# Kernel optimization log

Measured on AMD Instinct MI355X. Metric: run time of the kernel, lower is better.

The kernel has to match this reference:

```python
import jax, jax.numpy as jnp
import numpy as np
from jax import lax

DN = ('NCHW', 'OIHW', 'NCHW')
SAME = ((1, 1), (1, 1))
VALID = ((0, 0), (0, 0))


def conv(x, w, pad):
    return lax.conv_general_dilated(x, w, (1, 1), pad, dimension_numbers=DN)


def convT(x, w, strides):
    # inverse (transposed) conv; for kernel==stride this exactly inverts the
    # non-overlapping pooling rulebook used by spconv's SparseInverseConv2d
    return lax.conv_transpose(x, w, strides, 'VALID', dimension_numbers=DN)


def maxpool(x, k):
    return lax.reduce_window(x, -jnp.inf, lax.max, (1, 1) + k, (1, 1) + k, 'VALID')


def lrelu(x):
    return jnp.where(x >= 0, x, 0.01 * x)  # F.leaky_relu default slope


def setup_inputs() -> dict:
    key = jax.random.key(0)
    ks = jax.random.split(key, 14)
    B, C, H, W = 32, 6, 500, 128
    x = jax.random.normal(ks[0], (B, C, H, W), jnp.float32)  # fully dense => all voxels active

    def p(k, shape):
        return jax.random.normal(k, shape, jnp.float32) * 0.05

    return {
        'x': x,
        'w1': p(ks[1], (8, 6, 3, 3)),      # SubMConv2d 6->8
        'w2': p(ks[2], (16, 8, 3, 3)),     # SubMConv2d 8->16
        'w3': p(ks[3], (32, 16, 3, 3)),    # SubMConv2d 16->32
        'wmu': p(ks[4], (1, 32, 1, 5)),    # SparseConv2d 32->1, kernel (1,5)
        'wlv': p(ks[5], (1, 32, 1, 5)),
        'wu0': p(ks[6], (32, 1, 1, 5)),    # SparseInverseConv2d 1->32
        'wu1': p(ks[7], (32, 32, 5, 2)),   # inverse of pool3
        'w4': p(ks[8], (16, 32, 3, 3)),
        'wu2': p(ks[9], (16, 16, 5, 2)),   # inverse of pool2
        'w5': p(ks[10], (8, 16, 3, 3)),
        'wu3': p(ks[11], (8, 8, 2, 2)),    # inverse of pool1
        'w6': p(ks[12], (6, 8, 3, 3)),
    }


def reference(x, w1, w2, w3, wmu, wlv, wu0, wu1, w4, wu2, w5, wu3, w6):
    B = x.shape[0]
    # ---- encoder ----
    h = lrelu(conv(x, w1, SAME))        # [B,8,500,128]
    h = maxpool(h, (2, 2))              # [B,8,250,64]
    h = lrelu(conv(h, w2, SAME))        # [B,16,250,64]
    h = maxpool(h, (5, 2))              # [B,16,50,32]
    h = lrelu(conv(h, w3, SAME))        # [B,32,50,32]
    h = maxpool(h, (5, 2))              # [B,32,10,16]
    mu = conv(h, wmu, VALID)            # [B,1,10,12]
    logvar = conv(h, wlv, VALID)        # [B,1,10,12]
    # ---- reparameterise ----
    eps = jax.random.normal(jax.random.key(42), mu.shape, mu.dtype)
    z = mu + eps * jnp.exp(0.5 * logvar)
    # ---- decoder ----
    d = lrelu(convT(z, wu0, (1, 1)))    # [B,32,10,16]
    d = lrelu(convT(d, wu1, (5, 2)))    # [B,32,50,32]
    d = lrelu(conv(d, w4, SAME))        # [B,16,50,32]
    d = lrelu(convT(d, wu2, (5, 2)))    # [B,16,250,64]
    d = lrelu(conv(d, w5, SAME))        # [B,8,250,64]
    d = lrelu(convT(d, wu3, (2, 2)))    # [B,8,500,128]
    d = lrelu(conv(d, w6, SAME))        # [B,6,500,128]
    return (d, mu.reshape(B, -1), logvar.reshape(B, -1), z.reshape(B, -1))
```

## Files before the change

### kernel.cpp

```cpp
#include <hip/hip_runtime.h>
#include <stdint.h>

#define DI __device__ __forceinline__

DI float lrelu(float x){ return x >= 0.0f ? x : 0.01f*x; }

DI uint32_t rotl32(uint32_t x, int d){ return (x << d) | (x >> (32 - d)); }

DI void threefry_0_42(uint32_t& x0, uint32_t& x1){
  const uint32_t ks0 = 0u, ks1 = 42u, ks2 = 0x1BD11BF0u;
  x0 += ks0; x1 += ks1;
  #define TFR(d) { x0 += x1; x1 = rotl32(x1,(d)); x1 ^= x0; }
  TFR(13) TFR(15) TFR(26) TFR(6)  x0 += ks1; x1 += ks2 + 1u;
  TFR(17) TFR(29) TFR(16) TFR(24) x0 += ks2; x1 += ks0 + 2u;
  TFR(13) TFR(15) TFR(26) TFR(6)  x0 += ks0; x1 += ks1 + 3u;
  TFR(17) TFR(29) TFR(16) TFR(24) x0 += ks1; x1 += ks2 + 4u;
  TFR(13) TFR(15) TFR(26) TFR(6)  x0 += ks2; x1 += ks0 + 5u;
  #undef TFR
}

DI float erfinv_f32(float x){
  float w = -log1pf(-x*x);
  float p;
  if (w < 5.0f){
    w = w - 2.5f;
    p = 2.81022636e-08f;
    p = fmaf(p, w, 3.43273939e-07f);
    p = fmaf(p, w, -3.5233877e-06f);
    p = fmaf(p, w, -4.39150654e-06f);
    p = fmaf(p, w, 0.00021858087f);
    p = fmaf(p, w, -0.00125372503f);
    p = fmaf(p, w, -0.00417768164f);
    p = fmaf(p, w, 0.246640727f);
    p = fmaf(p, w, 1.50140941f);
  } else {
    w = sqrtf(w) - 3.0f;
    p = -0.000200214257f;
    p = fmaf(p, w, 0.000100950558f);
    p = fmaf(p, w, 0.00134934322f);
    p = fmaf(p, w, -0.00367342844f);
    p = fmaf(p, w, 0.00573950773f);
    p = fmaf(p, w, -0.0076224613f);
    p = fmaf(p, w, 0.00943887047f);
    p = fmaf(p, w, 1.00167406f);
    p = fmaf(p, w, 2.83297682f);
  }
  return p * x;
}

#define OUT_D_OFF   0
#define OUT_MU_OFF  12288000
#define OUT_LV_OFF  (12288000 + 3840)
#define OUT_Z_OFF   (12288000 + 7680)

__global__ __launch_bounds__(256) void k_enc1(const float* __restrict__ x,
                                              const float* __restrict__ w1,
                                              float* __restrict__ p1){
  __shared__ float tile[6*10*130];
  int tid = threadIdx.x;
  int band = blockIdx.x % 63;
  int b    = blockIdx.x / 63;
  int r0 = band*8;
  for (int idx = tid; idx < 6*10*130; idx += 256){
    int lc = idx % 130;
    int rest = idx / 130;
    int lr = rest % 10;
    int ch = rest / 10;
    int gr = r0 - 1 + lr, gc = lc - 1;
    float v = 0.0f;
    if ((unsigned)gr < 500u && (unsigned)gc < 128u)
      v = x[((b*6+ch)*500+gr)*128+gc];
    tile[idx] = v;
  }
  __syncthreads();
  int pw = tid & 63, pr = tid >> 6;
  int ph = band*4 + pr;
  float acc[2][2][8];
  #pragma unroll
  for (int a=0;a<2;a++)
    #pragma unroll
    for (int d=0;d<2;d++)
      #pragma unroll
      for (int o=0;o<8;o++) acc[a][d][o] = 0.0f;
  int base = (2*pr)*130 + 2*pw;
  #pragma unroll 2
  for (int c = 0; c < 6; ++c){
    float win[4][4];
    #pragma unroll
    for (int i=0;i<4;i++)
      #pragma unroll
      for (int j=0;j<4;j++)
        win[i][j] = tile[c*1300 + base + i*130 + j];
    #pragma unroll
    for (int kh=0;kh<3;kh++)
      #pragma unroll
      for (int kw=0;kw<3;kw++){
        float wv[8];
        #pragma unroll
        for (int o=0;o<8;o++) wv[o] = w1[((o*6+c)*3+kh)*3+kw];
        #pragma unroll
        for (int dy=0;dy<2;dy++)
          #pragma unroll
          for (int dx=0;dx<2;dx++){
            float v = win[dy+kh][dx+kw];
            #pragma unroll
            for (int o=0;o<8;o++) acc[dy][dx][o] = fmaf(v, wv[o], acc[dy][dx][o]);
          }
      }
  }
  if (ph < 250){
    #pragma unroll
    for (int o=0;o<8;o++){
      float m = fmaxf(fmaxf(acc[0][0][o], acc[0][1][o]), fmaxf(acc[1][0][o], acc[1][1][o]));
      p1[((b*8+o)*250+ph)*64+pw] = lrelu(m);
    }
  }
}

__global__ __launch_bounds__(256) void k_enc2(const float* __restrict__ in,
                                              const float* __restrict__ w2,
                                              float* __restrict__ p2){
  __shared__ float tile[8*22*66];
  int tid = threadIdx.x;
  int band = blockIdx.x % 13;
  int b    = blockIdx.x / 13;
  int r0 = band*20;
  for (int idx = tid; idx < 8*22*66; idx += 256){
    int lc = idx % 66;
    int rest = idx / 66;
    int lr = rest % 22;
    int ch = rest / 22;
    int gr = r0 - 1 + lr, gc = lc - 1;
    float v = 0.0f;
    if ((unsigned)gr < 250u && (unsigned)gc < 64u)
      v = in[((b*8+ch)*250+gr)*64+gc];
    tile[idx] = v;
  }
  __syncthreads();
  int dx = tid & 1; int u = tid >> 1;
  int pw = u & 31; int pr = (u >> 5) & 3;
  int cw = 2*pw + dx;
  int ph = band*4 + pr;
  float acc[5][16];
  #pragma unroll
  for (int dy=0;dy<5;dy++)
    #pragma unroll
    for (int o=0;o<16;o++) acc[dy][o] = 0.0f;
  int base = (5*pr)*66 + cw;
  #pragma unroll 1
  for (int c = 0; c < 8; ++c){
    float win[7][3];
    #pragma unroll
    for (int i=0;i<7;i++)
      #pragma unroll
      for (int j=0;j<3;j++)
        win[i][j] = tile[c*1452 + base + i*66 + j];
    #pragma unroll
    for (int kh=0;kh<3;kh++)
      #pragma unroll
      for (int kw=0;kw<3;kw++){
        float wv[16];
        #pragma unroll
        for (int o=0;o<16;o++) wv[o] = w2[((o*8+c)*3+kh)*3+kw];
        #pragma unroll
        for (int dy=0;dy<5;dy++){
          float v = win[dy+kh][kw];
          #pragma unroll
          for (int o=0;o<16;o++) acc[dy][o] = fmaf(v, wv[o], acc[dy][o]);
        }
      }
  }
  #pragma unroll
  for (int o=0;o<16;o++){
    float m = acc[0][o];
    #pragma unroll
    for (int dy=1;dy<5;dy++) m = fmaxf(m, acc[dy][o]);
    m = fmaxf(m, __shfl_xor(m, 1));
    if (dx == 0 && ph < 50) p2[((b*16+o)*50+ph)*32+pw] = lrelu(m);
  }
}

__global__ __launch_bounds__(256) void k_conv3(const float* __restrict__ in,
                                               const float* __restrict__ w3,
                                               float* __restrict__ outp){
  __shared__ float tile[16*10*34];
  int tid = threadIdx.x;
  int bi = blockIdx.x;
  int band = bi % 7; int oh = (bi/7) & 1; int b = bi / 14;
  int r0 = band*8;
  for (int idx = tid; idx < 16*10*34; idx += 256){
    int lc = idx % 34;
    int rest = idx / 34;
    int lr = rest % 10;
    int ch = rest / 10;
    int gr = r0 - 1 + lr, gc = lc - 1;
    float v = 0.0f;
    if ((unsigned)gr < 50u && (unsigned)gc < 32u)
      v = in[((b*16+ch)*50+gr)*32+gc];
    tile[idx] = v;
  }
  __syncthreads();
  int col = tid & 31, tr = tid >> 5;
  int h = r0 + tr;
  float acc[16];
  #pragma unroll
  for (int o=0;o<16;o++) acc[o] = 0.0f;
  int base = tr*34 + col;
  #pragma unroll 2
  for (int c = 0; c < 16; ++c){
    float win[3][3];
    #pragma unroll
    for (int i=0;i<3;i++)
      #pragma unroll
      for (int j=0;j<3;j++)
        win[i][j] = tile[c*340 + base + i*34 + j];
    #pragma unroll
    for (int kh=0;kh<3;kh++)
      #pragma unroll
      for (int kw=0;kw<3;kw++){
        float v = win[kh][kw];
        #pragma unroll
        for (int o=0;o<16;o++)
          acc[o] = fmaf(v, w3[(((oh*16+o)*16+c)*3+kh)*3+kw], acc[o]);
      }
  }
  if (h < 50){
    #pragma unroll
    for (int o=0;o<16;o++)
      outp[((b*32 + oh*16 + o)*50 + h)*32 + col] = lrelu(acc[o]);
  }
}

__global__ __launch_bounds__(256) void k_pool3(const float* __restrict__ in,
                                               float* __restrict__ outp){
  int t = blockIdx.x*256 + threadIdx.x;
  int pw = t & 15; int u = t >> 4; int ph = u % 10; u /= 10; int o = u & 31; int b = u >> 5;
  float m = -INFINITY;
  #pragma unroll
  for (int dh=0;dh<5;dh++)
    #pragma unroll
    for (int dw=0;dw<2;dw++)
      m = fmaxf(m, in[((b*32+o)*50 + 5*ph+dh)*32 + 2*pw+dw]);
  outp[((b*32+o)*10+ph)*16+pw] = m;
}

__global__ __launch_bounds__(256) void k_latent(const float* __restrict__ p3,
                                                const float* __restrict__ wmu,
                                                const float* __restrict__ wlv,
                                                float* __restrict__ outp){
  int t = blockIdx.x*256 + threadIdx.x;
  int w = t % 12; int h = (t/12) % 10; int b = t/120;
  float mu = 0.0f, lv = 0.0f;
  for (int c = 0; c < 32; ++c){
    const float* row = p3 + ((b*32+c)*10+h)*16 + w;
    #pragma unroll
    for (int kw=0;kw<5;kw++){
      float v = row[kw];
      mu = fmaf(v, wmu[c*5+kw], mu);
      lv = fmaf(v, wlv[c*5+kw], lv);
    }
  }
  uint32_t x0 = 0u, x1 = (uint32_t)t;
  threefry_0_42(x0, x1);
  uint32_t bits = x0 ^ x1;
  float f = __uint_as_float((bits >> 9) | 0x3f800000u) - 1.0f;
  const float lo = -0.99999994f;
  float uu = fmaxf(lo, f * 2.0f + lo);
  float eps = 1.41421356f * erfinv_f32(uu);
  float z = mu + eps * expf(0.5f * lv);
  outp[OUT_MU_OFF + t] = mu;
  outp[OUT_LV_OFF + t] = lv;
  outp[OUT_Z_OFF  + t] = z;
}

__global__ __launch_bounds__(256) void k_dec0(const float* __restrict__ outp,
                                              const float* __restrict__ wu0,
                                              float* __restrict__ d0){
  int t = blockIdx.x*256 + threadIdx.x;
  int w = t & 15; int u = t >> 4; int h = u % 10; u /= 10; int o = u & 31; int b = u >> 5;
  const float* z = outp + OUT_Z_OFF;
  float a = 0.0f;
  #pragma unroll
  for (int kw=0;kw<5;kw++){
    int ww = w + kw - 4;
    if ((unsigned)ww < 12u) a = fmaf(z[b*120 + h*12 + ww], wu0[o*5+kw], a);
  }
  d0[((b*32+o)*10+h)*16+w] = lrelu(a);
}

__global__ __launch_bounds__(256) void k_dec1(const float* __restrict__ d0,
                                              const float* __restrict__ wu1,
                                              float* __restrict__ d1){
  int t = blockIdx.x*256 + threadIdx.x;
  int wo = t & 31; int u = t >> 5; int ho = u % 50; u /= 50; int og = u & 3; int b = u >> 2;
  int i = ho / 5, r = ho - 5*i, jj = wo >> 1, s = wo & 1;
  const float* ip = d0 + b*5120 + i*16 + jj;
  float in[32];
  #pragma unroll
  for (int c=0;c<32;c++) in[c] = ip[c*160];
  #pragma unroll
  for (int oo=0;oo<8;oo++){
    int o = og*8 + oo;
    const float* wp = wu1 + (o*32*5 + (4-r))*2 + (1-s);
    float a = 0.0f;
    #pragma unroll
    for (int c=0;c<32;c++) a = fmaf(in[c], wp[c*10], a);
    d1[((b*32+o)*50+ho)*32+wo] = lrelu(a);
  }
}

__global__ __launch_bounds__(256) void k_c4(const float* __restrict__ in,
                                            const float* __restrict__ w4,
                                            float* __restrict__ outp){
  __shared__ float tile[32*10*34];
  int tid = threadIdx.x;
  int bi = blockIdx.x;
  int band = bi % 7; int oh = (bi/7) & 1; int b = bi / 14;
  int r0 = band*8;
  for (int idx = tid; idx < 32*10*34; idx += 256){
    int lc = idx % 34;
    int rest = idx / 34;
    int lr = rest % 10;
    int ch = rest / 10;
    int gr = r0 - 1 + lr, gc = lc - 1;
    float v = 0.0f;
    if ((unsigned)gr < 50u && (unsigned)gc < 32u)
      v = in[((b*32+ch)*50+gr)*32+gc];
    tile[idx] = v;
  }
  __syncthreads();
  int col = tid & 31, tr = tid >> 5;
  int h = r0 + tr;
  float acc[8];
  #pragma unroll
  for (int o=0;o<8;o++) acc[o] = 0.0f;
  int base = tr*34 + col;
  #pragma unroll 2
  for (int c = 0; c < 32; ++c){
    float win[3][3];
    #pragma unroll
    for (int i=0;i<3;i++)
      #pragma unroll
      for (int j=0;j<3;j++)
        win[i][j] = tile[c*340 + base + i*34 + j];
    #pragma unroll
    for (int kh=0;kh<3;kh++)
      #pragma unroll
      for (int kw=0;kw<3;kw++){
        float v = win[kh][kw];
        #pragma unroll
        for (int o=0;o<8;o++)
          acc[o] = fmaf(v, w4[(((oh*8+o)*32+c)*3+kh)*3+kw], acc[o]);
      }
  }
  if (h < 50){
    #pragma unroll
    for (int o=0;o<8;o++)
      outp[((b*16 + oh*8 + o)*50 + h)*32 + col] = lrelu(acc[o]);
  }
}

__global__ __launch_bounds__(256) void k_u2(const float* __restrict__ d2,
                                            const float* __restrict__ wu2,
                                            float* __restrict__ d3){
  int t = blockIdx.x*256 + threadIdx.x;
  int w = t & 63; int u = t >> 6; int h = u % 250; int b = u / 250;
  int i = h / 5, r = h - 5*i, jj = w >> 1, s = w & 1;
  const float* ip = d2 + b*25600 + i*32 + jj;
  float in[16];
  #pragma unroll
  for (int c=0;c<16;c++) in[c] = ip[c*1600];
  #pragma unroll
  for (int o=0;o<16;o++){
    const float* wp = wu2 + (o*16*5 + (4-r))*2 + (1-s);
    float a = 0.0f;
    #pragma unroll
    for (int c=0;c<16;c++) a = fmaf(in[c], wp[c*10], a);
    d3[((b*16+o)*250+h)*64+w] = lrelu(a);
  }
}

__global__ __launch_bounds__(256) void k_c5(const float* __restrict__ in,
                                            const float* __restrict__ w5,
                                            float* __restrict__ outp){
  __shared__ float tile[16*10*66];
  int tid = threadIdx.x;
  int band = blockIdx.x % 32;
  int b    = blockIdx.x / 32;
  int r0 = band*8;
  for (int idx = tid; idx < 16*10*66; idx += 256){
    int lc = idx % 66;
    int rest = idx / 66;
    int lr = rest % 10;
    int ch = rest / 10;
    int gr = r0 - 1 + lr, gc = lc - 1;
    float v = 0.0f;
    if ((unsigned)gr < 250u && (unsigned)gc < 64u)
      v = in[((b*16+ch)*250+gr)*64+gc];
    tile[idx] = v;
  }
  __syncthreads();
  int cp = tid & 31, tr = tid >> 5;
  int h = r0 + tr;
  float acc[2][8];
  #pragma unroll
  for (int dx=0;dx<2;dx++)
    #pragma unroll
    for (int o=0;o<8;o++) acc[dx][o] = 0.0f;
  int base = tr*66 + 2*cp;
  #pragma unroll 2
  for (int c = 0; c < 16; ++c){
    float win[3][4];
    #pragma unroll
    for (int i=0;i<3;i++)
      #pragma unroll
      for (int j=0;j<4;j++)
        win[i][j] = tile[c*660 + base + i*66 + j];
    #pragma unroll
    for (int kh=0;kh<3;kh++)
      #pragma unroll
      for (int kw=0;kw<3;kw++){
        float wv[8];
        #pragma unroll
        for (int o=0;o<8;o++) wv[o] = w5[((o*16+c)*3+kh)*3+kw];
        #pragma unroll
        for (int dx=0;dx<2;dx++){
          float v = win[kh][dx+kw];
          #pragma unroll
          for (int o=0;o<8;o++) acc[dx][o] = fmaf(v, wv[o], acc[dx][o]);
        }
      }
  }
  if (h < 250){
    #pragma unroll
    for (int dx=0;dx<2;dx++)
      #pragma unroll
      for (int o=0;o<8;o++)
        outp[((b*8+o)*250+h)*64 + 2*cp+dx] = lrelu(acc[dx][o]);
  }
}

__global__ __launch_bounds__(256) void k_u3c6(const float* __restrict__ d4,
                                              const float* __restrict__ wu3,
                                              const float* __restrict__ w6,
                                              float* __restrict__ outp){
  __shared__ __align__(16) float dt[8*10*132];
  __shared__ __align__(16) float wl[256];
  int tid = threadIdx.x;
  int band = blockIdx.x % 63;
  int b    = blockIdx.x / 63;
  int r0 = band*8;
  wl[tid] = wu3[tid];
  if (tid < 80){
    int ch = tid / 10, lr = tid % 10;
    dt[(ch*10+lr)*132 + 128] = 0.0f;
    dt[(ch*10+lr)*132 + 129] = 0.0f;
  }
  __syncthreads();
  for (int s = tid; s < 320; s += 256){
    int q = s & 31, lr = s >> 5;
    int h = r0 - 1 + lr;
    if ((unsigned)h < 500u){
      int i2 = h >> 1, r = h & 1;
      float2 dv[8];
      #pragma unroll
      for (int c=0;c<8;c++)
        dv[c] = *(const float2*)(d4 + ((b*8+c)*250 + i2)*64 + 2*q);
      int wbase = (1-r)*2;
      #pragma unroll
      for (int o5=0;o5<8;o5++){
        float a0=0.f,a1=0.f,a2=0.f,a3=0.f;
        #pragma unroll
        for (int c=0;c<8;c++){
          float2 wp = *(const float2*)(wl + o5*32 + c*4 + wbase);
          a0 = fmaf(dv[c].x, wp.y, a0);
          a1 = fmaf(dv[c].x, wp.x, a1);
          a2 = fmaf(dv[c].y, wp.y, a2);
          a3 = fmaf(dv[c].y, wp.x, a3);
        }
        float4 v4 = make_float4(lrelu(a0), lrelu(a1), lrelu(a2), lrelu(a3));
        *(float4*)(dt + (o5*10+lr)*132 + 4*q) = v4;
      }
    } else {
      float4 z = make_float4(0.f,0.f,0.f,0.f);
      #pragma unroll
      for (int o5=0;o5<8;o5++)
        *(float4*)(dt + (o5*10+lr)*132 + 4*q) = z;
    }
  }
  __syncthreads();
  int q = tid & 31, tr = tid >> 5;
  int R = r0 + tr;
  float acc[4][6];
  #pragma unroll
  for (int j=0;j<4;j++)
    #pragma unroll
    for (int o=0;o<6;o++) acc[j][o] = 0.0f;
  int left = (q==0) ? 129 : (4*q - 1);
  #pragma unroll 2
  for (int ch=0; ch<8; ++ch){
    #pragma unroll
    for (int wr=0; wr<3; ++wr){
      const float* row = dt + (ch*10 + tr + wr)*132;
      float win[6];
      float4 m = *(const float4*)(row + 4*q);
      win[0] = row[left];
      win[1] = m.x; win[2] = m.y; win[3] = m.z; win[4] = m.w;
      win[5] = row[4*q + 4];
      #pragma unroll
      for (int kw=0;kw<3;kw++){
        #pragma unroll
        for (int o=0;o<6;o++){
          float wv = w6[((o*8+ch)*3+wr)*3+kw];
          #pragma unroll
          for (int j=0;j<4;j++)
            acc[j][o] = fmaf(win[j+kw], wv, acc[j][o]);
        }
      }
    }
  }
  if (R < 500){
    #pragma unroll
    for (int o=0;o<6;o++){
      float4 v = make_float4(lrelu(acc[0][o]), lrelu(acc[1][o]),
                             lrelu(acc[2][o]), lrelu(acc[3][o]));
      *(float4*)(outp + ((b*6+o)*500 + R)*128 + 4*q) = v;
    }
  }
}

extern "C" void kernel_launch(void* const* d_in, const int* in_sizes, int n_in,
                              void* d_out, int out_size, void* d_ws, size_t ws_size,
                              hipStream_t stream){
  const float* x   = (const float*)d_in[0];
  const float* w1  = (const float*)d_in[1];
  const float* w2  = (const float*)d_in[2];
  const float* w3  = (const float*)d_in[3];
  const float* wmu = (const float*)d_in[4];
  const float* wlv = (const float*)d_in[5];
  const float* wu0 = (const float*)d_in[6];
  const float* wu1 = (const float*)d_in[7];
  const float* w4  = (const float*)d_in[8];
  const float* wu2 = (const float*)d_in[9];
  const float* w5  = (const float*)d_in[10];
  const float* wu3 = (const float*)d_in[11];
  const float* w6  = (const float*)d_in[12];
  float* out = (float*)d_out;
  float* A  = (float*)d_ws;
  float* Bb = A + 4096000;

  k_enc1 <<<2016, 256, 0, stream>>>(x,  w1,  A);
  k_enc2 <<< 416, 256, 0, stream>>>(A,  w2,  Bb);
  k_conv3<<< 448, 256, 0, stream>>>(Bb, w3,  A);
  k_pool3<<< 640, 256, 0, stream>>>(A,  Bb);
  k_latent<<< 15, 256, 0, stream>>>(Bb, wmu, wlv, out);
  k_dec0 <<< 640, 256, 0, stream>>>(out, wu0, A);
  k_dec1 <<< 800, 256, 0, stream>>>(A,  wu1, Bb);
  k_c4   <<< 448, 256, 0, stream>>>(Bb, w4,  A);
  k_u2   <<<2000, 256, 0, stream>>>(A,  wu2, Bb);
  k_c5   <<<1024, 256, 0, stream>>>(Bb, w5,  A);
  k_u3c6 <<<2016, 256, 0, stream>>>(A, wu3, w6, out);
}
```

Measured before the change: 381.0 us.

## Fuse pool3/latent/dec0/dec1 and u2 into c5; retile enc2 for more blocks

Merges pool3, the latent/reparameterisation step, dec0 and dec1 into one per-batch kernel that keeps its intermediates in shared memory. Also computes the u2 transposed conv inside the c5 tile load, so the large d3 intermediate is never written to or read from global memory. enc2 is retiled to 10-row bands with two output-channel groups, giving 800 blocks instead of 416. The fused latent kernel runs only 32 blocks with about 80KB of shared memory, so it may underuse the GPU. The u2c5 kernel also recomputes halo rows of u2.

```diff
diff --git a/kernel.cpp b/kernel.cpp
--- a/kernel.cpp
+++ b/kernel.cpp
@@ -120,63 +120,65 @@
 __global__ __launch_bounds__(256) void k_enc2(const float* __restrict__ in,
                                               const float* __restrict__ w2,
                                               float* __restrict__ p2){
-  __shared__ float tile[8*22*66];
+  __shared__ float tile[8*12*66];
   int tid = threadIdx.x;
-  int band = blockIdx.x % 13;
-  int b    = blockIdx.x / 13;
-  int r0 = band*20;
-  for (int idx = tid; idx < 8*22*66; idx += 256){
+  int band = blockIdx.x % 25;
+  int b    = blockIdx.x / 25;
+  int cr0 = band*10;
+  for (int idx = tid; idx < 8*12*66; idx += 256){
     int lc = idx % 66;
     int rest = idx / 66;
-    int lr = rest % 22;
-    int ch = rest / 22;
-    int gr = r0 - 1 + lr, gc = lc - 1;
+    int lr = rest % 12;
+    int ch = rest / 12;
+    int gr = cr0 - 1 + lr, gc = lc - 1;
     float v = 0.0f;
     if ((unsigned)gr < 250u && (unsigned)gc < 64u)
       v = in[((b*8+ch)*250+gr)*64+gc];
     tile[idx] = v;
   }
   __syncthreads();
-  int dx = tid & 1; int u = tid >> 1;
-  int pw = u & 31; int pr = (u >> 5) & 3;
+  int dx = tid & 1;
+  int pw = (tid >> 1) & 31;
+  int pr = (tid >> 6) & 1;
+  int og = tid >> 7;
   int cw = 2*pw + dx;
-  int ph = band*4 + pr;
-  float acc[5][16];
+  int ph = band*2 + pr;
+  float acc[5][8];
   #pragma unroll
   for (int dy=0;dy<5;dy++)
     #pragma unroll
-    for (int o=0;o<16;o++) acc[dy][o] = 0.0f;
+    for (int oo=0;oo<8;oo++) acc[dy][oo] = 0.0f;
   int base = (5*pr)*66 + cw;
-  #pragma unroll 1
+  #pragma unroll 2
   for (int c = 0; c < 8; ++c){
     float win[7][3];
     #pragma unroll
     for (int i=0;i<7;i++)
       #pragma unroll
       for (int j=0;j<3;j++)
-        win[i][j] = tile[c*1452 + base + i*66 + j];
+        win[i][j] = tile[c*792 + base + i*66 + j];
     #pragma unroll
     for (int kh=0;kh<3;kh++)
       #pragma unroll
       for (int kw=0;kw<3;kw++){
-        float wv[16];
-        #pragma unroll
-        for (int o=0;o<16;o++) wv[o] = w2[((o*8+c)*3+kh)*3+kw];
+        float wv[8];
+        #pragma unroll
+        for (int oo=0;oo<8;oo++) wv[oo] = w2[(((og*8+oo)*8+c)*3+kh)*3+kw];
         #pragma unroll
         for (int dy=0;dy<5;dy++){
           float v = win[dy+kh][kw];
           #pragma unroll
-          for (int o=0;o<16;o++) acc[dy][o] = fmaf(v, wv[o], acc[dy][o]);
+          for (int oo=0;oo<8;oo++) acc[dy][oo] = fmaf(v, wv[oo], acc[dy][oo]);
         }
       }
   }
   #pragma unroll
-  for (int o=0;o<16;o++){
-    float m = acc[0][o];
-    #pragma unroll
-    for (int dy=1;dy<5;dy++) m = fmaxf(m, acc[dy][o]);
+  for (int oo=0;oo<8;oo++){
+    float m = acc[0][oo];
+    #pragma unroll
+    for (int dy=1;dy<5;dy++) m = fmaxf(m, acc[dy][oo]);
     m = fmaxf(m, __shfl_xor(m, 1));
-    if (dx == 0 && ph < 50) p2[((b*16+o)*50+ph)*32+pw] = lrelu(m);
+    if (dx == 0) p2[((b*16+og*8+oo)*50+ph)*32+pw] = lrelu(m);
   }
 }
 
@@ -231,81 +233,85 @@
   }
 }
 
-__global__ __launch_bounds__(256) void k_pool3(const float* __restrict__ in,
-                                               float* __restrict__ outp){
-  int t = blockIdx.x*256 + threadIdx.x;
-  int pw = t & 15; int u = t >> 4; int ph = u % 10; u /= 10; int o = u & 31; int b = u >> 5;
-  float m = -INFINITY;
-  #pragma unroll
-  for (int dh=0;dh<5;dh++)
-    #pragma unroll
-    for (int dw=0;dw<2;dw++)
-      m = fmaxf(m, in[((b*32+o)*50 + 5*ph+dh)*32 + 2*pw+dw]);
-  outp[((b*32+o)*10+ph)*16+pw] = m;
-}
-
-__global__ __launch_bounds__(256) void k_latent(const float* __restrict__ p3,
+__global__ __launch_bounds__(256) void k_latdec(const float* __restrict__ h3,
                                                 const float* __restrict__ wmu,
                                                 const float* __restrict__ wlv,
-                                                float* __restrict__ outp){
-  int t = blockIdx.x*256 + threadIdx.x;
-  int w = t % 12; int h = (t/12) % 10; int b = t/120;
-  float mu = 0.0f, lv = 0.0f;
-  for (int c = 0; c < 32; ++c){
-    const float* row = p3 + ((b*32+c)*10+h)*16 + w;
+                                                const float* __restrict__ wu0,
+                                                const float* __restrict__ wu1,
+                                                float* __restrict__ outp,
+                                                float* __restrict__ d1){
+  __shared__ float p3s[5120];
+  __shared__ float zs[120];
+  __shared__ float d0s[5120];
+  __shared__ float w1s[10240];
+  int b = blockIdx.x, tid = threadIdx.x;
+  for (int i = tid; i < 10240; i += 256) w1s[i] = wu1[i];
+  for (int i = tid; i < 5120; i += 256){
+    int pw = i & 15; int u = i >> 4; int ph = u % 10; int c = u / 10;
+    const float* src = h3 + ((b*32+c)*50 + 5*ph)*32 + 2*pw;
+    float m = -INFINITY;
+    #pragma unroll
+    for (int dh=0;dh<5;dh++){
+      m = fmaxf(m, src[dh*32]);
+      m = fmaxf(m, src[dh*32+1]);
+    }
+    p3s[i] = m;
+  }
+  __syncthreads();
+  if (tid < 120){
+    int w = tid % 12, h = tid / 12;
+    float mu = 0.0f, lv = 0.0f;
+    for (int c = 0; c < 32; ++c){
+      const float* row = p3s + (c*10+h)*16 + w;
+      #pragma unroll
+      for (int kw=0;kw<5;kw++){
+        float v = row[kw];
+        mu = fmaf(v, wmu[c*5+kw], mu);
+        lv = fmaf(v, wlv[c*5+kw], lv);
+      }
+    }
+    int t = b*120 + tid;
+    uint32_t x0 = 0u, x1 = (uint32_t)t;
+    threefry_0_42(x0, x1);
+    uint32_t bits = x0 ^ x1;
+    float f = __uint_as_float((bits >> 9) | 0x3f800000u) - 1.0f;
+    const float lo = -0.99999994f;
+    float uu = fmaxf(lo, f * 2.0f + lo);
+    float eps = 1.41421356f * erfinv_f32(uu);
+    float z = mu + eps * expf(0.5f * lv);
+    outp[OUT_MU_OFF + t] = mu;
+    outp[OUT_LV_OFF + t] = lv;
+    outp[OUT_Z_OFF  + t] = z;
+    zs[tid] = z;
+  }
+  __syncthreads();
+  for (int i = tid; i < 5120; i += 256){
+    int w = i & 15; int u = i >> 4; int h = u % 10; int o = u / 10;
+    float a = 0.0f;
     #pragma unroll
     for (int kw=0;kw<5;kw++){
-      float v = row[kw];
-      mu = fmaf(v, wmu[c*5+kw], mu);
-      lv = fmaf(v, wlv[c*5+kw], lv);
-    }
-  }
-  uint32_t x0 = 0u, x1 = (uint32_t)t;
-  threefry_0_42(x0, x1);
-  uint32_t bits = x0 ^ x1;
-  float f = __uint_as_float((bits >> 9) | 0x3f800000u) - 1.0f;
-  const float lo = -0.99999994f;
-  float uu = fmaxf(lo, f * 2.0f + lo);
-  float eps = 1.41421356f * erfinv_f32(uu);
-  float z = mu + eps * expf(0.5f * lv);
-  outp[OUT_MU_OFF + t] = mu;
-  outp[OUT_LV_OFF + t] = lv;
-  outp[OUT_Z_OFF  + t] = z;
-}
-
-__global__ __launch_bounds__(256) void k_dec0(const float* __restrict__ outp,
-                                              const float* __restrict__ wu0,
-                                              float* __restrict__ d0){
-  int t = blockIdx.x*256 + threadIdx.x;
-  int w = t & 15; int u = t >> 4; int h = u % 10; u /= 10; int o = u & 31; int b = u >> 5;
-  const float* z = outp + OUT_Z_OFF;
-  float a = 0.0f;
-  #pragma unroll
-  for (int kw=0;kw<5;kw++){
-    int ww = w + kw - 4;
-    if ((unsigned)ww < 12u) a = fmaf(z[b*120 + h*12 + ww], wu0[o*5+kw], a);
-  }
-  d0[((b*32+o)*10+h)*16+w] = lrelu(a);
-}
-
-__global__ __launch_bounds__(256) void k_dec1(const float* __restrict__ d0,
-                                              const float* __restrict__ wu1,
-                                              float* __restrict__ d1){
-  int t = blockIdx.x*256 + threadIdx.x;
-  int wo = t & 31; int u = t >> 5; int ho = u % 50; u /= 50; int og = u & 3; int b = u >> 2;
-  int i = ho / 5, r = ho - 5*i, jj = wo >> 1, s = wo & 1;
-  const float* ip = d0 + b*5120 + i*16 + jj;
-  float in[32];
-  #pragma unroll
-  for (int c=0;c<32;c++) in[c] = ip[c*160];
-  #pragma unroll
-  for (int oo=0;oo<8;oo++){
-    int o = og*8 + oo;
-    const float* wp = wu1 + (o*32*5 + (4-r))*2 + (1-s);
-    float a = 0.0f;
-    #pragma unroll
-    for (int c=0;c<32;c++) a = fmaf(in[c], wp[c*10], a);
-    d1[((b*32+o)*50+ho)*32+wo] = lrelu(a);
+      int ww = w + kw - 4;
+      if ((unsigned)ww < 12u) a = fmaf(zs[h*12 + ww], wu0[o*5+kw], a);
+    }
+    d0s[i] = lrelu(a);
+  }
+  __syncthreads();
+  for (int it = 0; it < 25; ++it){
+    int idx = tid + 256*it;
+    int wo = idx & 31; int u = idx >> 5; int ho = u % 50; int og = u / 50;
+    int i5 = ho / 5, r = ho - 5*i5, jj = wo >> 1, s = wo & 1;
+    float inv[32];
+    #pragma unroll
+    for (int c=0;c<32;c++) inv[c] = d0s[(c*10+i5)*16 + jj];
+    int wb = (4-r)*2 + (1-s);
+    #pragma unroll
+    for (int oo=0;oo<8;oo++){
+      int o = og*8 + oo;
+      float a = 0.0f;
+      #pragma unroll
+      for (int c=0;c<32;c++) a = fmaf(inv[c], w1s[o*320 + c*10 + wb], a);
+      d1[((b*32+o)*50+ho)*32+wo] = lrelu(a);
+    }
   }
 }
 
@@ -360,44 +366,44 @@
   }
 }
 
-__global__ __launch_bounds__(256) void k_u2(const float* __restrict__ d2,
-                                            const float* __restrict__ wu2,
-                                            float* __restrict__ d3){
-  int t = blockIdx.x*256 + threadIdx.x;
-  int w = t & 63; int u = t >> 6; int h = u % 250; int b = u / 250;
-  int i = h / 5, r = h - 5*i, jj = w >> 1, s = w & 1;
-  const float* ip = d2 + b*25600 + i*32 + jj;
-  float in[16];
-  #pragma unroll
-  for (int c=0;c<16;c++) in[c] = ip[c*1600];
-  #pragma unroll
-  for (int o=0;o<16;o++){
-    const float* wp = wu2 + (o*16*5 + (4-r))*2 + (1-s);
-    float a = 0.0f;
-    #pragma unroll
-    for (int c=0;c<16;c++) a = fmaf(in[c], wp[c*10], a);
-    d3[((b*16+o)*250+h)*64+w] = lrelu(a);
-  }
-}
-
-__global__ __launch_bounds__(256) void k_c5(const float* __restrict__ in,
-                                            const float* __restrict__ w5,
-                                            float* __restrict__ outp){
-  __shared__ float tile[16*10*66];
+__global__ __launch_bounds__(256) void k_u2c5(const float* __restrict__ d2,
+                                              const float* __restrict__ wu2,
+                                              const float* __restrict__ w5,
+                                              float* __restrict__ d4out){
+  __shared__ float dt[16*10*66];
+  __shared__ float d2s[16*3*32];
+  __shared__ float w2s[2560];
   int tid = threadIdx.x;
-  int band = blockIdx.x % 32;
-  int b    = blockIdx.x / 32;
+  int band = blockIdx.x & 31;
+  int b    = blockIdx.x >> 5;
   int r0 = band*8;
-  for (int idx = tid; idx < 16*10*66; idx += 256){
-    int lc = idx % 66;
-    int rest = idx / 66;
-    int lr = rest % 10;
-    int ch = rest / 10;
-    int gr = r0 - 1 + lr, gc = lc - 1;
+  int i0 = (r0 == 0) ? 0 : (r0-1)/5;
+  for (int i = tid; i < 2560; i += 256) w2s[i] = wu2[i];
+  for (int idx = tid; idx < 1536; idx += 256){
+    int jj = idx & 31; int u = idx >> 5; int di = u % 3; int cc = u / 3;
+    int i5 = i0 + di;
+    d2s[cc*96 + di*32 + jj] = (i5 < 50) ? d2[((b*16+cc)*50 + i5)*32 + jj] : 0.0f;
+  }
+  __syncthreads();
+  for (int s = tid; s < 10560; s += 256){
+    int lc = s % 66;
+    int u = s / 66;
+    int lr = u % 10;
+    int c  = u / 10;
+    int gc = lc - 1;
+    int h  = r0 - 1 + lr;
     float v = 0.0f;
-    if ((unsigned)gr < 250u && (unsigned)gc < 64u)
-      v = in[((b*16+ch)*250+gr)*64+gc];
-    tile[idx] = v;
+    if ((unsigned)h < 250u && (unsigned)gc < 64u){
+      int i5 = h / 5, r = h - 5*i5, jj = gc >> 1, sx = gc & 1;
+      int di = i5 - i0;
+      const float* dp = d2s + di*32 + jj;
+      const float* wp = w2s + c*160 + (4-r)*2 + (1-sx);
+      float a = 0.0f;
+      #pragma unroll
+      for (int cc=0;cc<16;cc++) a = fmaf(dp[cc*96], wp[cc*10], a);
+      v = lrelu(a);
+    }
+    dt[s] = v;
   }
   __syncthreads();
   int cp = tid & 31, tr = tid >> 5;
@@ -415,7 +421,7 @@
     for (int i=0;i<3;i++)
       #pragma unroll
       for (int j=0;j<4;j++)
-        win[i][j] = tile[c*660 + base + i*66 + j];
+        win[i][j] = dt[c*660 + base + i*66 + j];
     #pragma unroll
     for (int kh=0;kh<3;kh++)
       #pragma unroll
@@ -436,7 +442,7 @@
     for (int dx=0;dx<2;dx++)
       #pragma unroll
       for (int o=0;o<8;o++)
-        outp[((b*8+o)*250+h)*64 + 2*cp+dx] = lrelu(acc[dx][o]);
+        d4out[((b*8+o)*250+h)*64 + 2*cp+dx] = lrelu(acc[dx][o]);
   }
 }
 
@@ -550,14 +556,10 @@
   float* Bb = A + 4096000;
 
   k_enc1 <<<2016, 256, 0, stream>>>(x,  w1,  A);
-  k_enc2 <<< 416, 256, 0, stream>>>(A,  w2,  Bb);
+  k_enc2 <<< 800, 256, 0, stream>>>(A,  w2,  Bb);
   k_conv3<<< 448, 256, 0, stream>>>(Bb, w3,  A);
-  k_pool3<<< 640, 256, 0, stream>>>(A,  Bb);
-  k_latent<<< 15, 256, 0, stream>>>(Bb, wmu, wlv, out);
-  k_dec0 <<< 640, 256, 0, stream>>>(out, wu0, A);
-  k_dec1 <<< 800, 256, 0, stream>>>(A,  wu1, Bb);
+  k_latdec<<<  32, 256, 0, stream>>>(A, wmu, wlv, wu0, wu1, out, Bb);
   k_c4   <<< 448, 256, 0, stream>>>(Bb, w4,  A);
-  k_u2   <<<2000, 256, 0, stream>>>(A,  wu2, Bb);
-  k_c5   <<<1024, 256, 0, stream>>>(Bb, w5,  A);
-  k_u3c6 <<<2016, 256, 0, stream>>>(A, wu3, w6, out);
-}
+  k_u2c5 <<<1024, 256, 0, stream>>>(A,  wu2, w5, Bb);
+  k_u3c6 <<<2016, 256, 0, stream>>>(Bb, wu3, w6, out);
+}
```

Result: slower. 403.1 us (+5.8%).
